# Performance work log

Measured on AMD Instinct MI355X. Metric: run time of the kernel, lower is better.

## Reference

```python
import jax, jax.numpy as jnp
import numpy as np

N = 50000          # num nodes
E = 256            # expert_hidden_dim
H = 512            # hidden_dim (expert output / GNN dim)
NE = 5             # num experts: action, spatial, temporal, semantic, safety
K = 2              # top_k
GH = 128           # gating hidden dim
EDGES = 800000
L = 2              # gnn layers
TEMP = 1.0


def setup_inputs() -> dict:
    key = jax.random.key(0)
    ks = jax.random.split(key, 16)
    s = 0.02
    inp = {
        "text": jax.random.normal(ks[0], (N, E), jnp.float32),
        "tabular": jax.random.normal(ks[1], (N, E), jnp.float32),
        "structured": jax.random.normal(ks[2], (N, E), jnp.float32),
        "edge_index": jax.random.randint(ks[3], (2, EDGES), 0, N, jnp.int64),
        # gating MLP: [3E] -> GH -> NE
        "Wg1": jax.random.normal(ks[4], (3 * E, GH), jnp.float32) * s,
        "bg1": jnp.zeros((GH,), jnp.float32),
        "Wg2": jax.random.normal(ks[5], (GH, NE), jnp.float32) * s,
        "bg2": jnp.zeros((NE,), jnp.float32),
        # 5 expert MLPs (stacked): E -> H -> H
        "We1": jax.random.normal(ks[6], (NE, E, H), jnp.float32) * s,
        "be1": jnp.zeros((NE, H), jnp.float32),
        "We2": jax.random.normal(ks[7], (NE, H, H), jnp.float32) * s,
        "be2": jnp.zeros((NE, H), jnp.float32),
        # GNN per-layer self/neighbor transforms
        "Wself": jax.random.normal(ks[8], (L, H, H), jnp.float32) * s,
        "Wnbr": jax.random.normal(ks[9], (L, H, H), jnp.float32) * s,
    }
    return inp


def _moe_gnn(text, tabular, structured, edge_index,
             Wg1, bg1, Wg2, bg2, We1, be1, We2, be2, Wself, Wnbr):
    # ---- gating: softmax over experts, top-k, renormalize ----
    combined = jnp.concatenate([text, tabular, structured], axis=-1)  # [N, 3E]
    g = jax.nn.relu(combined @ Wg1 + bg1)
    logits = (g @ Wg2 + bg2) / TEMP                                   # [N, NE]
    probs = jax.nn.softmax(logits, axis=-1)
    top_vals, top_idx = jax.lax.top_k(probs, K)                       # [N, K]
    gates = top_vals / jnp.sum(top_vals, axis=-1, keepdims=True)      # [N, K]

    # ---- expert inputs per the forward() mapping ----
    # action->tabular, spatial->structured, temporal->text, semantic->text, safety->structured
    xin = jnp.stack([tabular, structured, text, text, structured])    # [NE, N, E]

    # ---- expert MLPs (all experts computed densely, selected by gather) ----
    h1 = jax.nn.gelu(jnp.einsum('end,edh->enh', xin, We1) + be1[:, None, :])
    eout = jnp.einsum('enh,eho->eno', h1, We2) + be2[:, None, :]      # [NE, N, H]

    # ---- gather-dispatch-scatter: weighted sum of top-k expert outputs ----
    sel = eout[top_idx, jnp.arange(N)[:, None], :]                    # [N, K, H]
    node_feats = jnp.sum(gates[..., None] * sel, axis=1)              # [N, H]

    # ---- GNN message passing over edge list ----
    src, dst = edge_index[0], edge_index[1]
    h = node_feats
    for l in range(L):
        msg = jax.ops.segment_sum((h @ Wnbr[l])[src], dst, num_segments=N)
        h = jax.nn.relu(h @ Wself[l] + msg)
    return h


def reference(text, tabular, structured, edge_index,
              Wg1, bg1, Wg2, bg2, We1, be1, We2, be2, Wself, Wnbr):
    return _moe_gnn(text, tabular, structured, edge_index,
                    Wg1, bg1, Wg2, bg2, We1, be1, We2, be2, Wself, Wnbr)
```

## Files before the change

kernel.cpp:

```cpp
#include <hip/hip_runtime.h>
#include <hip/hip_bf16.h>

#define NNODE 50000
#define M_PAD 50048
#define EDIM  256
#define HDIM  512
#define NEXP  5
#define GHID  128
#define NEDGE 800000
#define SLOTCAP 101504
#define MAXT_ALL 792
#define MAXT_R   396

typedef __attribute__((ext_vector_type(8))) short  short8;
typedef __attribute__((ext_vector_type(4))) float  float4v;
typedef __attribute__((ext_vector_type(4))) unsigned short ushort4v;

typedef __attribute__((address_space(1))) const unsigned int gas_u32;
typedef __attribute__((address_space(3))) unsigned int       las_u32;

__device__ __forceinline__ void gl_lds16(const unsigned short* g, unsigned short* l) {
    __builtin_amdgcn_global_load_lds((gas_u32*)g, (las_u32*)l, 16, 0, 0);
}
__device__ __forceinline__ unsigned short f2b(float f) {
    unsigned u = __builtin_bit_cast(unsigned, f);
    u += 0x7FFFu + ((u >> 16) & 1u);
    return (unsigned short)(u >> 16);
}
__device__ __forceinline__ float b2f(unsigned short h) {
    unsigned u = ((unsigned)h) << 16;
    return __builtin_bit_cast(float, u);
}
__device__ __forceinline__ float fast_tanh(float y) {
    float ay = fabsf(y);
    float e  = __expf(-2.0f * ay);
    float t  = (1.0f - e) / (1.0f + e);
    return (y < 0.0f) ? -t : t;
}
__device__ __forceinline__ float gelu_tanh(float x) {
    float inner = 0.7978845608028654f * (x + 0.044715f * x * x * x);
    return 0.5f * x * (1.0f + fast_tanh(inner));
}

#define WP_N0 655360
#define WP_C1 1966080
#define WP_C2 3014656
#define WP_TOT 3112960
#define WP_T_RL  WP_TOT
#define WP_T_DEG (WP_TOT + SLOTCAP)
#define WP_T_SC  (WP_TOT + SLOTCAP + NNODE)
#define WP_ALL   (WP_TOT + SLOTCAP + NNODE + 16)
__global__ __launch_bounds__(256) void wprep(
    const float* __restrict__ We1, const float* __restrict__ We2,
    const float* __restrict__ Wself, const float* __restrict__ Wnbr,
    const float* __restrict__ Wg1,
    unsigned short* __restrict__ We1t, unsigned short* __restrict__ We2t,
    unsigned short* __restrict__ Wcat0, unsigned short* __restrict__ Wcat1,
    unsigned short* __restrict__ Wg1h, unsigned short* __restrict__ Wg1l,
    int* __restrict__ rowlist, int* __restrict__ deg, int* __restrict__ slotcnt) {
    for (int i = blockIdx.x * blockDim.x + threadIdx.x; i < WP_ALL;
         i += gridDim.x * blockDim.x) {
        if (i < WP_N0) {
            int b = i >> 17, rem = i & 131071;
            int c = rem >> 8, r = rem & 255;
            We1t[i] = f2b(We1[(size_t)b * 131072 + (size_t)r * 512 + c]);
        } else if (i < WP_C1) {
            int j = i - WP_N0;
            int b = j >> 18, rem = j & 262143;
            int c = rem >> 9, r = rem & 511;
            We2t[j] = f2b(We2[(size_t)b * 262144 + (size_t)r * 512 + c]);
        } else if (i < WP_C2) {
            int j = i - WP_C1;
            int qd = j >> 18, k = j & 262143;
            int c = k >> 9, r = k & 511;
            const float* in = (qd & 1) ? Wnbr : Wself;
            if (qd >> 1) in += 262144;
            unsigned short* out = (qd >> 1) ? Wcat1 : Wcat0;
            int ko = (qd & 1) * 512;
            out[(size_t)c * 1024 + ko + r] = f2b(in[(size_t)r * 512 + c]);
        } else if (i < WP_TOT) {
            int j = i - WP_C2;
            int c = j / 768, r = j - c * 768;
            float f = Wg1[(size_t)r * 128 + c];
            unsigned short hi = f2b(f);
            Wg1h[j] = hi;
            Wg1l[j] = f2b(f - b2f(hi));
        } else if (i < WP_T_DEG) {
            rowlist[i - WP_T_RL] = -1;
        } else if (i < WP_T_SC) {
            deg[i - WP_T_DEG] = 0;
        } else {
            slotcnt[i - WP_T_SC] = 0;
        }
    }
}

__global__ __launch_bounds__(256) void gate128(
    const float* __restrict__ xtxt, const float* __restrict__ xtab, const float* __restrict__ xstr,
    const unsigned short* __restrict__ Bh, const unsigned short* __restrict__ Blo,
    const float* __restrict__ bg1, float* __restrict__ g) {
    __shared__ unsigned short Ash[128 * 64];
    __shared__ unsigned short Asl[128 * 64];
    __shared__ unsigned short Bsh[128 * 64];
    __shared__ unsigned short Bsl[128 * 64];
    const int t = threadIdx.x, w = t >> 6, lane = t & 63;
    const int ln = lane & 15, q = lane >> 4;
    const int wm = (w >> 1) * 64, wn = (w & 1) * 64;
    const int rb = w * 8 + (lane >> 3), kg = lane & 7;
    const int koff = (kg ^ (rb & 7)) * 8;
    const float* xs[3] = { xtxt, xtab, xstr };
    const unsigned short* Bgh = Bh  + (size_t)rb * 768 + koff;
    const unsigned short* Bgl = Blo + (size_t)rb * 768 + koff;
    unsigned short* Blh = &Bsh[rb * 64 + kg * 8];
    unsigned short* Bll = &Bsl[rb * 64 + kg * 8];
    float4v acc[4][4];
#pragma unroll
    for (int i = 0; i < 4; ++i)
#pragma unroll
        for (int j = 0; j < 4; ++j) acc[i][j] = (float4v){0.f, 0.f, 0.f, 0.f};

    for (int kt = 0; kt < 768; kt += 64) {
        const float* xp = xs[kt >> 8];
        const int kloc = kt & 255;
        __syncthreads();
#pragma unroll
        for (int it = 0; it < 4; ++it) {
            int row = blockIdx.y * 128 + rb + 32 * it;
            union { short8 v; unsigned short s[8]; } ph, pl;
            if (row < NNODE) {
                const float* sp = xp + (size_t)row * EDIM + kloc + koff;
                float4v a0 = *(const float4v*)sp;
                float4v a1 = *(const float4v*)(sp + 4);
#pragma unroll
                for (int c = 0; c < 4; ++c) {
                    unsigned short h0 = f2b(a0[c]);
                    ph.s[c] = h0; pl.s[c] = f2b(a0[c] - b2f(h0));
                    unsigned short h1 = f2b(a1[c]);
                    ph.s[4 + c] = h1; pl.s[4 + c] = f2b(a1[c] - b2f(h1));
                }
            } else {
#pragma unroll
                for (int c = 0; c < 8; ++c) { ph.s[c] = 0; pl.s[c] = 0; }
            }
            *(short8*)&Ash[(rb + 32 * it) * 64 + kg * 8] = ph.v;
            *(short8*)&Asl[(rb + 32 * it) * 64 + kg * 8] = pl.v;
            gl_lds16(Bgh + (size_t)it * 32 * 768 + kt, Blh + it * 32 * 64);
            gl_lds16(Bgl + (size_t)it * 32 * 768 + kt, Bll + it * 32 * 64);
        }
        __syncthreads();
#pragma unroll
        for (int kk = 0; kk < 2; ++kk) {
            short8 ah[4], al[4], bh[4], bl[4];
#pragma unroll
            for (int i = 0; i < 4; ++i) {
                int off = (wm + 16 * i + ln) * 64 + (((kk * 4 + q) ^ (ln & 7)) * 8);
                ah[i] = *(const short8*)&Ash[off];
                al[i] = *(const short8*)&Asl[off];
            }
#pragma unroll
            for (int j = 0; j < 4; ++j) {
                int off = (wn + 16 * j + ln) * 64 + (((kk * 4 + q) ^ (ln & 7)) * 8);
                bh[j] = *(const short8*)&Bsh[off];
                bl[j] = *(const short8*)&Bsl[off];
            }
#pragma unroll
            for (int i = 0; i < 4; ++i)
#pragma unroll
                for (int j = 0; j < 4; ++j) {
                    acc[i][j] = __builtin_amdgcn_mfma_f32_16x16x32_bf16(ah[i], bh[j], acc[i][j], 0, 0, 0);
                    acc[i][j] = __builtin_amdgcn_mfma_f32_16x16x32_bf16(ah[i], bl[j], acc[i][j], 0, 0, 0);
                    acc[i][j] = __builtin_amdgcn_mfma_f32_16x16x32_bf16(al[i], bh[j], acc[i][j], 0, 0, 0);
                }
        }
    }
    const int gm0 = blockIdx.y * 128 + wm;
#pragma unroll
    for (int i = 0; i < 4; ++i)
#pragma unroll
        for (int j = 0; j < 4; ++j) {
            int gn = wn + 16 * j + ln;
            float bc = bg1[gn];
#pragma unroll
            for (int r = 0; r < 4; ++r) {
                int gm = gm0 + 16 * i + q * 4 + r;
                g[(size_t)gm * GHID + gn] = fmaxf(acc[i][j][r] + bc, 0.f);
            }
        }
}

__global__ __launch_bounds__(256) void gating(
    const float* __restrict__ g, const float* __restrict__ Wg2, const float* __restrict__ bg2,
    float* __restrict__ gates, int* __restrict__ esel) {
    int wv = threadIdx.x >> 6, lane = threadIdx.x & 63;
    int n = blockIdx.x * 4 + wv;
    float p[NEXP];
    float g1 = g[(size_t)n * GHID + lane];
    float g2 = g[(size_t)n * GHID + 64 + lane];
#pragma unroll
    for (int e = 0; e < NEXP; ++e)
        p[e] = g1 * Wg2[lane * NEXP + e] + g2 * Wg2[(64 + lane) * NEXP + e];
#pragma unroll
    for (int off = 32; off > 0; off >>= 1)
#pragma unroll
        for (int e = 0; e < NEXP; ++e) p[e] += __shfl_xor(p[e], off, 64);
    if (lane == 0) {
        float l[NEXP], mx = -1e30f;
#pragma unroll
        for (int e = 0; e < NEXP; ++e) { l[e] = p[e] + bg2[e]; mx = fmaxf(mx, l[e]); }
        float pr[NEXP], s = 0.f;
#pragma unroll
        for (int e = 0; e < NEXP; ++e) { pr[e] = expf(l[e] - mx); s += pr[e]; }
#pragma unroll
        for (int e = 0; e < NEXP; ++e) pr[e] /= s;
        int i0 = 0;
#pragma unroll
        for (int e = 1; e < NEXP; ++e) if (pr[e] > pr[i0]) i0 = e;
        int i1 = -1;
#pragma unroll
        for (int e = 0; e < NEXP; ++e) if (e != i0 && (i1 < 0 || pr[e] > pr[i1])) i1 = e;
        float v0 = pr[i0], v1 = pr[i1], s2 = v0 + v1;
        gates[2 * n]     = v0 / s2;
        gates[2 * n + 1] = v1 / s2;
        esel[2 * n]      = i0;
        esel[2 * n + 1]  = i1;
    }
}

__global__ __launch_bounds__(256) void slot_count(const int* __restrict__ esel,
                                                  int* __restrict__ slotcnt) {
    __shared__ int h[10];
    if (threadIdx.x < 10) h[threadIdx.x] = 0;
    __syncthreads();
    int n = blockIdx.x * 256 + threadIdx.x;
    if (n < NNODE) {
        atomicAdd(&h[esel[2 * n] * 2 + 0], 1);
        atomicAdd(&h[esel[2 * n + 1] * 2 + 1], 1);
    }
    __syncthreads();
    if (threadIdx.x < 10) atomicAdd(&slotcnt[threadIdx.x], h[threadIdx.x]);
}
__global__ void seg_plan(const int* __restrict__ slotcnt, int* __restrict__ cursor,
                         int* __restrict__ header, int2* __restrict__ meta_all,
                         int2* __restrict__ meta_r0, int2* __restrict__ meta_r1) {
    if (threadIdx.x == 0 && blockIdx.x == 0) {
        int base = 0, ta = 0, t0 = 0, t1 = 0;
        for (int s = 0; s < 10; ++s) {
            cursor[s] = base;
            int nt = (slotcnt[s] + 127) >> 7;
            for (int k = 0; k < nt; ++k) {
                int2 m; m.x = s; m.y = base + k * 128;
                meta_all[ta++] = m;
                if (s & 1) meta_r1[t1++] = m; else meta_r0[t0++] = m;
            }
            base += nt * 128;
        }
        header[0] = ta; header[1] = t0; header[2] = t1;
    }
}
__global__ __launch_bounds__(256) void slot_fill(
    const int* __restrict__ esel, const float* __restrict__ gates, int* __restrict__ cursor,
    int* __restrict__ rowlist, float* __restrict__ gateval) {
    __shared__ int h[10], base[10];
    if (threadIdx.x < 10) h[threadIdx.x] = 0;
    __syncthreads();
    int n = blockIdx.x * 256 + threadIdx.x;
    int s0 = 0, s1 = 0, p0 = 0, p1 = 0;
    bool on = (n < NNODE);
    if (on) {
        s0 = esel[2 * n] * 2;
        s1 = esel[2 * n + 1] * 2 + 1;
        p0 = atomicAdd(&h[s0], 1);
        p1 = atomicAdd(&h[s1], 1);
    }
    __syncthreads();
    if (threadIdx.x < 10) base[threadIdx.x] = atomicAdd(&cursor[threadIdx.x], h[threadIdx.x]);
    __syncthreads();
    if (on) {
        int q0 = base[s0] + p0, q1 = base[s1] + p1;
        rowlist[q0] = n; gateval[q0] = gates[2 * n];
        rowlist[q1] = n; gateval[q1] = gates[2 * n + 1];
    }
}

__global__ __launch_bounds__(256) void gemm_moe1(
    const float* __restrict__ xtab, const float* __restrict__ xstr, const float* __restrict__ xtxt,
    const unsigned short* __restrict__ We1t, const float* __restrict__ be1,
    const int* __restrict__ header, const int2* __restrict__ meta,
    const int* __restrict__ rowlist, unsigned short* __restrict__ h1) {
    const int wg = blockIdx.x;
    const int xcd = wg & 7, s = wg >> 3;
    const int mt_i = (s >> 2) * 8 + xcd;
    const int ntile = s & 3;
    if (mt_i >= header[0]) return;
    __shared__ unsigned short As[128 * 64];
    __shared__ unsigned short Bs[128 * 64];
    int2 mt = meta[mt_i];
    const int eid = mt.x >> 1, rowbase = mt.y;
    const float* xf = (eid == 0) ? xtab : ((eid == 1 || eid == 4) ? xstr : xtxt);
    const int t = threadIdx.x, w = t >> 6, lane = t & 63;
    const int ln = lane & 15, q = lane >> 4;
    const int wm = (w >> 1) * 64, wn = (w & 1) * 64;
    const int rb = w * 8 + (lane >> 3), kg = lane & 7;
    const int koff = (kg ^ (rb & 7)) * 8;
    int rows[4];
#pragma unroll
    for (int it = 0; it < 4; ++it) {
        int rr = rowlist[rowbase + rb + 32 * it];
        rows[it] = (rr < 0) ? 0 : rr;
    }
    const unsigned short* Bg = We1t + (size_t)eid * HDIM * EDIM
                             + (size_t)(ntile * 128 + rb) * EDIM + koff;
    unsigned short* Bl = &Bs[rb * 64 + kg * 8];
    float4v acc[4][4];
#pragma unroll
    for (int i = 0; i < 4; ++i)
#pragma unroll
        for (int j = 0; j < 4; ++j) acc[i][j] = (float4v){0.f, 0.f, 0.f, 0.f};

    for (int kt = 0; kt < EDIM; kt += 64) {
        __syncthreads();
#pragma unroll
        for (int it = 0; it < 4; ++it) {
            const float* sp = xf + (size_t)rows[it] * EDIM + kt + koff;
            float4v a0 = *(const float4v*)sp;
            float4v a1 = *(const float4v*)(sp + 4);
            union { short8 v; unsigned short s[8]; } pk;
#pragma unroll
            for (int c = 0; c < 4; ++c) { pk.s[c] = f2b(a0[c]); pk.s[4 + c] = f2b(a1[c]); }
            *(short8*)&As[(rb + 32 * it) * 64 + kg * 8] = pk.v;
            gl_lds16(Bg + (size_t)it * 32 * EDIM + kt, Bl + it * 32 * 64);
        }
        __syncthreads();
#pragma unroll
        for (int kk = 0; kk < 2; ++kk) {
            short8 af[4], bf[4];
#pragma unroll
            for (int i = 0; i < 4; ++i)
                af[i] = *(const short8*)&As[(wm + 16 * i + ln) * 64 + (((kk * 4 + q) ^ (ln & 7)) * 8)];
#pragma unroll
            for (int j = 0; j < 4; ++j)
                bf[j] = *(const short8*)&Bs[(wn + 16 * j + ln) * 64 + (((kk * 4 + q) ^ (ln & 7)) * 8)];
#pragma unroll
            for (int i = 0; i < 4; ++i)
#pragma unroll
                for (int j = 0; j < 4; ++j)
                    acc[i][j] = __builtin_amdgcn_mfma_f32_16x16x32_bf16(af[i], bf[j], acc[i][j], 0, 0, 0);
        }
    }
    const int gn0 = ntile * 128 + wn;
#pragma unroll
    for (int i = 0; i < 4; ++i)
#pragma unroll
        for (int j = 0; j < 4; ++j) {
            int gn = gn0 + 16 * j + ln;
            float bc = be1[eid * HDIM + gn];
#pragma unroll
            for (int r = 0; r < 4; ++r) {
                int slot = rowbase + wm + 16 * i + q * 4 + r;
                h1[(size_t)slot * HDIM + gn] = f2b(gelu_tanh(acc[i][j][r] + bc));
            }
        }
}

template<int RMW>
__global__ __launch_bounds__(256) void gemm_moe2(
    const unsigned short* __restrict__ h1, const unsigned short* __restrict__ We2t,
    const float* __restrict__ be2, const int* __restrict__ header,
    const int2* __restrict__ meta, const int* __restrict__ rowlist,
    const float* __restrict__ gateval, unsigned short* __restrict__ nf) {
    const int wg = blockIdx.x;
    const int xcd = wg & 7, s = wg >> 3;
    const int mt_i = (s >> 2) * 8 + xcd;
    const int ntile = s & 3;
    if (mt_i >= header[RMW ? 2 : 1]) return;
    __shared__ unsigned short As[128 * 64];
    __shared__ unsigned short Bs[128 * 64];
    int2 mt = meta[mt_i];
    const int eid = mt.x >> 1, rowbase = mt.y;
    const int t = threadIdx.x, w = t >> 6, lane = t & 63;
    const int ln = lane & 15, q = lane >> 4;
    const int wm = (w >> 1) * 64, wn = (w & 1) * 64;
    const int rb = w * 8 + (lane >> 3), kg = lane & 7;
    const int koff = (kg ^ (rb & 7)) * 8;
    const unsigned short* Ag = h1 + (size_t)(rowbase + rb) * HDIM + koff;
    const unsigned short* Bg = We2t + (size_t)eid * HDIM * HDIM
                             + (size_t)(ntile * 128 + rb) * HDIM + koff;
    unsigned short* Al = &As[rb * 64 + kg * 8];
    unsigned short* Bl = &Bs[rb * 64 + kg * 8];
    float4v acc[4][4];
#pragma unroll
    for (int i = 0; i < 4; ++i)
#pragma unroll
        for (int j = 0; j < 4; ++j) acc[i][j] = (float4v){0.f, 0.f, 0.f, 0.f};

    for (int kt = 0; kt < HDIM; kt += 64) {
        __syncthreads();
#pragma unroll
        for (int it = 0; it < 4; ++it) {
            gl_lds16(Ag + (size_t)it * 32 * HDIM + kt, Al + it * 32 * 64);
            gl_lds16(Bg + (size_t)it * 32 * HDIM + kt, Bl + it * 32 * 64);
        }
        __syncthreads();
#pragma unroll
        for (int kk = 0; kk < 2; ++kk) {
            short8 af[4], bf[4];
#pragma unroll
            for (int i = 0; i < 4; ++i)
                af[i] = *(const short8*)&As[(wm + 16 * i + ln) * 64 + (((kk * 4 + q) ^ (ln & 7)) * 8)];
#pragma unroll
            for (int j = 0; j < 4; ++j)
                bf[j] = *(const short8*)&Bs[(wn + 16 * j + ln) * 64 + (((kk * 4 + q) ^ (ln & 7)) * 8)];
#pragma unroll
            for (int i = 0; i < 4; ++i)
#pragma unroll
                for (int j = 0; j < 4; ++j)
                    acc[i][j] = __builtin_amdgcn_mfma_f32_16x16x32_bf16(af[i], bf[j], acc[i][j], 0, 0, 0);
        }
    }
    const int gn0 = ntile * 128 + wn;
#pragma unroll
    for (int i = 0; i < 4; ++i)
#pragma unroll
        for (int r = 0; r < 4; ++r) {
            int slot = rowbase + wm + 16 * i + q * 4 + r;
            int node = rowlist[slot];
            if (node >= 0) {
                float gt = gateval[slot];
#pragma unroll
                for (int j = 0; j < 4; ++j) {
                    int gn = gn0 + 16 * j + ln;
                    size_t o = (size_t)node * HDIM + gn;
                    float v = gt * (acc[i][j][r] + be2[eid * HDIM + gn]);
                    nf[o] = RMW ? f2b(b2f(nf[o]) + v) : f2b(v);
                }
            }
        }
}

#define GNN_MT (M_PAD / 128)
template<int FINAL>
__global__ __launch_bounds__(256) void gemm_gnn(
    const unsigned short* __restrict__ A0, const unsigned short* __restrict__ A1,
    const unsigned short* __restrict__ Bt, unsigned short* __restrict__ Cb,
    float* __restrict__ Cf) {
    const int wg = blockIdx.x;
    const int xcd = wg & 7, s = wg >> 3;
    const int mt = (s >> 2) * 8 + xcd;
    const int ntile = s & 3;
    if (mt >= GNN_MT) return;
    __shared__ unsigned short As[128 * 64];
    __shared__ unsigned short Bs[128 * 64];
    const int t = threadIdx.x, w = t >> 6, lane = t & 63;
    const int ln = lane & 15, q = lane >> 4;
    const int wm = (w >> 1) * 64, wn = (w & 1) * 64;
    const int rb = w * 8 + (lane >> 3), kg = lane & 7;
    const int koff = (kg ^ (rb & 7)) * 8;
    const unsigned short* Ag0 = A0 + (size_t)(mt * 128 + rb) * HDIM + koff;
    const unsigned short* Ag1 = A1 + (size_t)(mt * 128 + rb) * HDIM + koff;
    const unsigned short* Bg  = Bt + (size_t)(ntile * 128 + rb) * 1024 + koff;
    unsigned short* Al = &As[rb * 64 + kg * 8];
    unsigned short* Bl = &Bs[rb * 64 + kg * 8];
    float4v acc[4][4];
#pragma unroll
    for (int i = 0; i < 4; ++i)
#pragma unroll
        for (int j = 0; j < 4; ++j) acc[i][j] = (float4v){0.f, 0.f, 0.f, 0.f};

    for (int kt = 0; kt < 1024; kt += 64) {
        __syncthreads();
#pragma unroll
        for (int it = 0; it < 4; ++it) {
            const unsigned short* asrc = (kt < HDIM)
                ? (Ag0 + (size_t)it * 32 * HDIM + kt)
                : (Ag1 + (size_t)it * 32 * HDIM + (kt - HDIM));
            gl_lds16(asrc, Al + it * 32 * 64);
            gl_lds16(Bg + (size_t)it * 32 * 1024 + kt, Bl + it * 32 * 64);
        }
        __syncthreads();
#pragma unroll
        for (int kk = 0; kk < 2; ++kk) {
            short8 af[4], bf[4];
#pragma unroll
            for (int i = 0; i < 4; ++i)
                af[i] = *(const short8*)&As[(wm + 16 * i + ln) * 64 + (((kk * 4 + q) ^ (ln & 7)) * 8)];
#pragma unroll
            for (int j = 0; j < 4; ++j)
                bf[j] = *(const short8*)&Bs[(wn + 16 * j + ln) * 64 + (((kk * 4 + q) ^ (ln & 7)) * 8)];
#pragma unroll
            for (int i = 0; i < 4; ++i)
#pragma unroll
                for (int j = 0; j < 4; ++j)
                    acc[i][j] = __builtin_amdgcn_mfma_f32_16x16x32_bf16(af[i], bf[j], acc[i][j], 0, 0, 0);
        }
    }
    const int gm0 = mt * 128 + wm;
    const int gn0 = ntile * 128 + wn;
#pragma unroll
    for (int i = 0; i < 4; ++i)
#pragma unroll
        for (int j = 0; j < 4; ++j) {
            int gn = gn0 + 16 * j + ln;
#pragma unroll
            for (int r = 0; r < 4; ++r) {
                int gm = gm0 + 16 * i + q * 4 + r;
                float v = fmaxf(acc[i][j][r], 0.f);
                if (FINAL) {
                    if (gm < NNODE) Cf[(size_t)gm * HDIM + gn] = v;
                } else {
                    Cb[(size_t)gm * HDIM + gn] = f2b(v);
                }
            }
        }
}

__global__ void hist_kernel(const int* __restrict__ dst, int* __restrict__ deg) {
    int i = blockIdx.x * blockDim.x + threadIdx.x;
    if (i < NEDGE) atomicAdd(&deg[dst[i]], 1);
}
__global__ void scan_block(const int* __restrict__ in, int* __restrict__ incl,
                           int* __restrict__ bsum, int n) {
    __shared__ int s[256];
    int i = blockIdx.x * 256 + threadIdx.x;
    s[threadIdx.x] = (i < n) ? in[i] : 0;
    __syncthreads();
    for (int off = 1; off < 256; off <<= 1) {
        int t = (threadIdx.x >= (unsigned)off) ? s[threadIdx.x - off] : 0;
        __syncthreads();
        s[threadIdx.x] += t;
        __syncthreads();
    }
    if (i < n) incl[i] = s[threadIdx.x];
    if (bsum != nullptr && threadIdx.x == 255) bsum[blockIdx.x] = s[255];
}
__global__ void scan_fix(const int* __restrict__ incl, const int* __restrict__ deg,
                         const int* __restrict__ bscan, int* __restrict__ rowstart,
                         int* __restrict__ ecur) {
    int i = blockIdx.x * blockDim.x + threadIdx.x;
    if (i < NNODE) {
        int b = i >> 8;
        int add = (b > 0) ? bscan[b - 1] : 0;
        int st = incl[i] - deg[i] + add;
        rowstart[i] = st;
        ecur[i] = st;
    }
}
__global__ void fill_csr(const int* __restrict__ src, const int* __restrict__ dst,
                         int* __restrict__ ecur, int* __restrict__ srcs) {
    int e = blockIdx.x * blockDim.x + threadIdx.x;
    if (e < NEDGE) {
        int pos = atomicAdd(&ecur[dst[e]], 1);
        srcs[pos] = src[e];
    }
}

__global__ __launch_bounds__(256) void msg_sum_w(
    const unsigned short* __restrict__ h, const int* __restrict__ rowstart,
    const int* __restrict__ deg, const int* __restrict__ srcs,
    unsigned short* __restrict__ agg) {
    const int wv = threadIdx.x >> 6, lane = threadIdx.x & 63;
    const int n = blockIdx.x * 4 + wv;
    const int st = rowstart[n], d = deg[n];
    float acc[8] = {0.f,0.f,0.f,0.f,0.f,0.f,0.f,0.f};
    const unsigned short* hp = h + (size_t)lane * 8;
    for (int cb = 0; cb < d; cb += 64) {
        int cnt = d - cb; if (cnt > 64) cnt = 64;
        int sidx = (cb + lane < d) ? srcs[st + cb + lane] : 0;
        int t = 0;
        for (; t + 4 <= cnt; t += 4) {
            int s0 = __shfl(sidx, t,     64);
            int s1 = __shfl(sidx, t + 1, 64);
            int s2 = __shfl(sidx, t + 2, 64);
            int s3 = __shfl(sidx, t + 3, 64);
            short8 v0 = *(const short8*)(hp + (size_t)s0 * HDIM);
            short8 v1 = *(const short8*)(hp + (size_t)s1 * HDIM);
            short8 v2 = *(const short8*)(hp + (size_t)s2 * HDIM);
            short8 v3 = *(const short8*)(hp + (size_t)s3 * HDIM);
#pragma unroll
            for (int c = 0; c < 8; ++c)
                acc[c] += (b2f((unsigned short)v0[c]) + b2f((unsigned short)v1[c]))
                        + (b2f((unsigned short)v2[c]) + b2f((unsigned short)v3[c]));
        }
        for (; t < cnt; ++t) {
            int s = __shfl(sidx, t, 64);
            short8 v = *(const short8*)(hp + (size_t)s * HDIM);
#pragma unroll
            for (int c = 0; c < 8; ++c) acc[c] += b2f((unsigned short)v[c]);
        }
    }
    union { short8 v; unsigned short s[8]; } o;
#pragma unroll
    for (int c = 0; c < 8; ++c) o.s[c] = f2b(acc[c]);
    *(short8*)(agg + (size_t)n * HDIM + lane * 8) = o.v;
}

extern "C" void kernel_launch(void* const* d_in, const int* in_sizes, int n_in,
                              void* d_out, int out_size, void* d_ws, size_t ws_size,
                              hipStream_t stream) {
    (void)in_sizes; (void)n_in; (void)out_size; (void)ws_size;
    const float* text       = (const float*)d_in[0];
    const float* tabular    = (const float*)d_in[1];
    const float* structured = (const float*)d_in[2];
    const int*   e_in       = (const int*)d_in[3];
    const float* Wg1  = (const float*)d_in[4];
    const float* bg1  = (const float*)d_in[5];
    const float* Wg2  = (const float*)d_in[6];
    const float* bg2  = (const float*)d_in[7];
    const float* We1  = (const float*)d_in[8];
    const float* be1  = (const float*)d_in[9];
    const float* We2  = (const float*)d_in[10];
    const float* be2  = (const float*)d_in[11];
    const float* Wself = (const float*)d_in[12];
    const float* Wnbr  = (const float*)d_in[13];
    const int* src = e_in;
    const int* dst = e_in + NEDGE;
    float* dout = (float*)d_out;

    char* w = (char*)d_ws;
    auto alloc = [&](size_t bytes) { char* p = w; w += (bytes + 511) & ~(size_t)511; return p; };
    const size_t SZ_H = (size_t)M_PAD * HDIM * 2;
    unsigned short* We1t  = (unsigned short*)alloc((size_t)NEXP * HDIM * EDIM * 2);
    unsigned short* We2t  = (unsigned short*)alloc((size_t)NEXP * HDIM * HDIM * 2);
    unsigned short* Wcat0 = (unsigned short*)alloc((size_t)HDIM * 1024 * 2);
    unsigned short* Wcat1 = (unsigned short*)alloc((size_t)HDIM * 1024 * 2);
    unsigned short* Wg1h  = (unsigned short*)alloc((size_t)GHID * 768 * 2);
    unsigned short* Wg1l  = (unsigned short*)alloc((size_t)GHID * 768 * 2);
    float* gates    = (float*)alloc((size_t)NNODE * 2 * 4);
    int*   esel     = (int*)alloc((size_t)NNODE * 2 * 4);
    int*   slotcnt  = (int*)alloc(16 * 4);
    int*   scursor  = (int*)alloc(16 * 4);
    int*   header   = (int*)alloc(16 * 4);
    int2*  meta_all = (int2*)alloc((size_t)MAXT_ALL * 8);
    int2*  meta_r0  = (int2*)alloc((size_t)MAXT_R * 8);
    int2*  meta_r1  = (int2*)alloc((size_t)MAXT_R * 8);
    int*   rowlist  = (int*)alloc((size_t)SLOTCAP * 4);
    float* gateval  = (float*)alloc((size_t)SLOTCAP * 4);
    int*   deg      = (int*)alloc((size_t)NNODE * 4);
    int*   incl     = (int*)alloc((size_t)NNODE * 4);
    int*   bsum     = (int*)alloc(1024 * 4);
    int*   bscan    = (int*)alloc(1024 * 4);
    int*   rowstart = (int*)alloc((size_t)NNODE * 4);
    int*   ecur     = (int*)alloc((size_t)NNODE * 4);
    int*   srcs     = (int*)alloc((size_t)NEDGE * 4);
    unsigned short* nfb = (unsigned short*)alloc(SZ_H);
    char* regA = alloc((size_t)M_PAD * GHID * 4 > SZ_H ? (size_t)M_PAD * GHID * 4 : SZ_H);
    float*          gbuf = (float*)regA;
    unsigned short* aggb = (unsigned short*)regA;
    char* regB = alloc((size_t)SLOTCAP * HDIM * 2);
    unsigned short* h1c = (unsigned short*)regB;
    unsigned short* hb  = (unsigned short*)regB;

    wprep<<<1024, 256, 0, stream>>>(We1, We2, Wself, Wnbr, Wg1,
                                    We1t, We2t, Wcat0, Wcat1, Wg1h, Wg1l,
                                    rowlist, deg, slotcnt);

    gate128<<<dim3(1, M_PAD / 128), 256, 0, stream>>>(text, tabular, structured,
                                                      Wg1h, Wg1l, bg1, gbuf);
    gating<<<NNODE / 4, 256, 0, stream>>>(gbuf, Wg2, bg2, gates, esel);

    slot_count<<<(NNODE + 255) / 256, 256, 0, stream>>>(esel, slotcnt);
    seg_plan<<<1, 64, 0, stream>>>(slotcnt, scursor, header, meta_all, meta_r0, meta_r1);
    slot_fill<<<(NNODE + 255) / 256, 256, 0, stream>>>(esel, gates, scursor, rowlist, gateval);

    gemm_moe1<<<MAXT_ALL * 4, 256, 0, stream>>>(
        tabular, structured, text, We1t, be1, header, meta_all, rowlist, h1c);
    gemm_moe2<0><<<8 * 50 * 4, 256, 0, stream>>>(
        h1c, We2t, be2, header, meta_r0, rowlist, gateval, nfb);
    gemm_moe2<1><<<8 * 50 * 4, 256, 0, stream>>>(
        h1c, We2t, be2, header, meta_r1, rowlist, gateval, nfb);

    const int NB = (NNODE + 255) / 256;
    hist_kernel<<<(NEDGE + 255) / 256, 256, 0, stream>>>(dst, deg);
    scan_block<<<NB, 256, 0, stream>>>(deg, incl, bsum, NNODE);
    scan_block<<<1, 256, 0, stream>>>(bsum, bscan, nullptr, NB);
    scan_fix<<<NB, 256, 0, stream>>>(incl, deg, bscan, rowstart, ecur);
    fill_csr<<<(NEDGE + 255) / 256, 256, 0, stream>>>(src, dst, ecur, srcs);

    msg_sum_w<<<NNODE / 4, 256, 0, stream>>>(nfb, rowstart, deg, srcs, aggb);
    gemm_gnn<0><<<8 * 49 * 4, 256, 0, stream>>>(nfb, aggb, Wcat0, hb, nullptr);

    msg_sum_w<<<NNODE / 4, 256, 0, stream>>>(hb, rowstart, deg, srcs, aggb);
    gemm_gnn<1><<<8 * 49 * 4, 256, 0, stream>>>(hb, aggb, Wcat1, nullptr, dout);
}
```

Baseline: 1.048 ms.

## Bucket CSR edges by source quarter and split gather by feature slice per XCD

Builds the CSR with four buckets per destination node, keyed by which quarter of the source-node range the edge comes from. The neighbour-sum kernel then walks the quarters in order and assigns 128-column feature slices to XCD pairs, so each gather phase touches a smaller, more cache-resident slice of h. The aim is better L2/MALL hit rates on the random gathers. The cost is a 4x larger degree/scan array, a new second-level scan kernel, serial per-thread edge loops with less memory-level parallelism, and a dependence on blocks being dispatched round-robin across XCDs.

```diff
diff --git a/kernel.cpp b/kernel.cpp
--- a/kernel.cpp
+++ b/kernel.cpp
@@ -41,6 +41,9 @@
     float inner = 0.7978845608028654f * (x + 0.044715f * x * x * x);
     return 0.5f * x * (1.0f + fast_tanh(inner));
 }
+__device__ __forceinline__ int quarter(int s) {
+    return (s >= 25000) ? ((s >= 37500) ? 3 : 2) : ((s >= 12500) ? 1 : 0);
+}
 
 #define WP_N0 655360
 #define WP_C1 1966080
@@ -48,8 +51,8 @@
 #define WP_TOT 3112960
 #define WP_T_RL  WP_TOT
 #define WP_T_DEG (WP_TOT + SLOTCAP)
-#define WP_T_SC  (WP_TOT + SLOTCAP + NNODE)
-#define WP_ALL   (WP_TOT + SLOTCAP + NNODE + 16)
+#define WP_T_SC  (WP_TOT + SLOTCAP + 4 * NNODE)
+#define WP_ALL   (WP_TOT + SLOTCAP + 4 * NNODE + 16)
 __global__ __launch_bounds__(256) void wprep(
     const float* __restrict__ We1, const float* __restrict__ We2,
     const float* __restrict__ Wself, const float* __restrict__ Wnbr,
@@ -57,7 +60,7 @@
     unsigned short* __restrict__ We1t, unsigned short* __restrict__ We2t,
     unsigned short* __restrict__ Wcat0, unsigned short* __restrict__ Wcat1,
     unsigned short* __restrict__ Wg1h, unsigned short* __restrict__ Wg1l,
-    int* __restrict__ rowlist, int* __restrict__ deg, int* __restrict__ slotcnt) {
+    int* __restrict__ rowlist, int* __restrict__ deg4, int* __restrict__ slotcnt) {
     for (int i = blockIdx.x * blockDim.x + threadIdx.x; i < WP_ALL;
          i += gridDim.x * blockDim.x) {
         if (i < WP_N0) {
@@ -88,7 +91,7 @@
         } else if (i < WP_T_DEG) {
             rowlist[i - WP_T_RL] = -1;
         } else if (i < WP_T_SC) {
-            deg[i - WP_T_DEG] = 0;
+            deg4[i - WP_T_DEG] = 0;
         } else {
             slotcnt[i - WP_T_SC] = 0;
         }
@@ -513,9 +516,10 @@
         }
 }
 
-__global__ void hist_kernel(const int* __restrict__ dst, int* __restrict__ deg) {
+__global__ void hist4(const int* __restrict__ src, const int* __restrict__ dst,
+                      int* __restrict__ deg4) {
     int i = blockIdx.x * blockDim.x + threadIdx.x;
-    if (i < NEDGE) atomicAdd(&deg[dst[i]], 1);
+    if (i < NEDGE) atomicAdd(&deg4[4 * dst[i] + quarter(src[i])], 1);
 }
 __global__ void scan_block(const int* __restrict__ in, int* __restrict__ incl,
                            int* __restrict__ bsum, int n) {
@@ -532,65 +536,92 @@
     if (i < n) incl[i] = s[threadIdx.x];
     if (bsum != nullptr && threadIdx.x == 255) bsum[blockIdx.x] = s[255];
 }
-__global__ void scan_fix(const int* __restrict__ incl, const int* __restrict__ deg,
-                         const int* __restrict__ bscan, int* __restrict__ rowstart,
-                         int* __restrict__ ecur) {
+__global__ void scan_lvl2(const int* __restrict__ in, int* __restrict__ out, int n) {
+    __shared__ int s[1024];
+    int i = threadIdx.x;
+    s[i] = (i < n) ? in[i] : 0;
+    __syncthreads();
+    for (int off = 1; off < 1024; off <<= 1) {
+        int t = (i >= (unsigned)off) ? s[i - off] : 0;
+        __syncthreads();
+        s[i] += t;
+        __syncthreads();
+    }
+    if (i < n) out[i] = s[i];
+}
+__global__ void scan_fix4(const int* __restrict__ incl, const int* __restrict__ deg4,
+                          const int* __restrict__ bscan, int* __restrict__ rowstart4,
+                          int* __restrict__ ecur4, int n) {
     int i = blockIdx.x * blockDim.x + threadIdx.x;
-    if (i < NNODE) {
+    if (i < n) {
         int b = i >> 8;
         int add = (b > 0) ? bscan[b - 1] : 0;
-        int st = incl[i] - deg[i] + add;
-        rowstart[i] = st;
-        ecur[i] = st;
-    }
-}
-__global__ void fill_csr(const int* __restrict__ src, const int* __restrict__ dst,
-                         int* __restrict__ ecur, int* __restrict__ srcs) {
+        int st = incl[i] - deg4[i] + add;
+        rowstart4[i] = st;
+        ecur4[i] = st;
+    }
+}
+__global__ void fill_csr4(const int* __restrict__ src, const int* __restrict__ dst,
+                          int* __restrict__ ecur4, int* __restrict__ srcs) {
     int e = blockIdx.x * blockDim.x + threadIdx.x;
     if (e < NEDGE) {
-        int pos = atomicAdd(&ecur[dst[e]], 1);
-        srcs[pos] = src[e];
-    }
-}
-
-__global__ __launch_bounds__(256) void msg_sum_w(
-    const unsigned short* __restrict__ h, const int* __restrict__ rowstart,
-    const int* __restrict__ deg, const int* __restrict__ srcs,
+        int s = src[e];
+        int pos = atomicAdd(&ecur4[4 * dst[e] + quarter(s)], 1);
+        srcs[pos] = s;
+    }
+}
+
+#define MSQ_NPB 64
+#define MSQ_CHUNKS ((NNODE + MSQ_NPB - 1) / MSQ_NPB)
+#define MSQ_GRID (8 * ((MSQ_CHUNKS + 1) / 2))
+__global__ __launch_bounds__(256) void msg_sum_q(
+    const unsigned short* __restrict__ h, const int* __restrict__ rowstart4,
+    const int* __restrict__ deg4, const int* __restrict__ srcs,
     unsigned short* __restrict__ agg) {
-    const int wv = threadIdx.x >> 6, lane = threadIdx.x & 63;
-    const int n = blockIdx.x * 4 + wv;
-    const int st = rowstart[n], d = deg[n];
-    float acc[8] = {0.f,0.f,0.f,0.f,0.f,0.f,0.f,0.f};
-    const unsigned short* hp = h + (size_t)lane * 8;
-    for (int cb = 0; cb < d; cb += 64) {
-        int cnt = d - cb; if (cnt > 64) cnt = 64;
-        int sidx = (cb + lane < d) ? srcs[st + cb + lane] : 0;
-        int t = 0;
-        for (; t + 4 <= cnt; t += 4) {
-            int s0 = __shfl(sidx, t,     64);
-            int s1 = __shfl(sidx, t + 1, 64);
-            int s2 = __shfl(sidx, t + 2, 64);
-            int s3 = __shfl(sidx, t + 3, 64);
-            short8 v0 = *(const short8*)(hp + (size_t)s0 * HDIM);
-            short8 v1 = *(const short8*)(hp + (size_t)s1 * HDIM);
-            short8 v2 = *(const short8*)(hp + (size_t)s2 * HDIM);
-            short8 v3 = *(const short8*)(hp + (size_t)s3 * HDIM);
-#pragma unroll
-            for (int c = 0; c < 8; ++c)
-                acc[c] += (b2f((unsigned short)v0[c]) + b2f((unsigned short)v1[c]))
-                        + (b2f((unsigned short)v2[c]) + b2f((unsigned short)v3[c]));
-        }
-        for (; t < cnt; ++t) {
-            int s = __shfl(sidx, t, 64);
-            short8 v = *(const short8*)(hp + (size_t)s * HDIM);
-#pragma unroll
-            for (int c = 0; c < 8; ++c) acc[c] += b2f((unsigned short)v[c]);
-        }
-    }
-    union { short8 v; unsigned short s[8]; } o;
-#pragma unroll
-    for (int c = 0; c < 8; ++c) o.s[c] = f2b(acc[c]);
-    *(short8*)(agg + (size_t)n * HDIM + lane * 8) = o.v;
+    const int blk = blockIdx.x;
+    const int xcd = blk & 7, j = blk >> 3;
+    const int slice = xcd >> 1;
+    const int chunk = j * 2 + (xcd & 1);
+    if (chunk >= MSQ_CHUNKS) return;
+    const int slot = threadIdx.x >> 4;
+    const int slane = threadIdx.x & 15;
+    const int nbase = chunk * MSQ_NPB;
+    const unsigned short* hs = h + slice * 128 + slane * 8;
+    float acc[4][8];
+#pragma unroll
+    for (int d = 0; d < 4; ++d)
+#pragma unroll
+        for (int c = 0; c < 8; ++c) acc[d][c] = 0.f;
+#pragma unroll 1
+    for (int q = 0; q < 4; ++q) {
+#pragma unroll
+        for (int d = 0; d < 4; ++d) {
+            int n = nbase + d * 16 + slot;
+            if (n >= NNODE) continue;
+            int st = rowstart4[4 * n + q];
+            int dg = deg4[4 * n + q];
+            if (dg <= 0) continue;
+            int s = srcs[st];
+            for (int t = 0; t < dg; ++t) {
+                int snext = (t + 1 < dg) ? srcs[st + t + 1] : 0;
+                short8 v = *(const short8*)(hs + (size_t)s * HDIM);
+#pragma unroll
+                for (int c = 0; c < 8; ++c) acc[d][c] += b2f((unsigned short)v[c]);
+                s = snext;
+            }
+        }
+    }
+#pragma unroll
+    for (int d = 0; d < 4; ++d) {
+        int n = nbase + d * 16 + slot;
+        if (n < NNODE) {
+            union { short8 v; unsigned short s[8]; } o;
+#pragma unroll
+            for (int c = 0; c < 8; ++c) o.s[c] = f2b(acc[d][c]);
+            __builtin_nontemporal_store(o.v,
+                (short8*)(agg + (size_t)n * HDIM + slice * 128 + slane * 8));
+        }
+    }
 }
 
 extern "C" void kernel_launch(void* const* d_in, const int* in_sizes, int n_in,
@@ -634,12 +665,12 @@
     int2*  meta_r1  = (int2*)alloc((size_t)MAXT_R * 8);
     int*   rowlist  = (int*)alloc((size_t)SLOTCAP * 4);
     float* gateval  = (float*)alloc((size_t)SLOTCAP * 4);
-    int*   deg      = (int*)alloc((size_t)NNODE * 4);
-    int*   incl     = (int*)alloc((size_t)NNODE * 4);
+    int*   deg4     = (int*)alloc((size_t)4 * NNODE * 4);
+    int*   incl     = (int*)alloc((size_t)4 * NNODE * 4);
     int*   bsum     = (int*)alloc(1024 * 4);
     int*   bscan    = (int*)alloc(1024 * 4);
-    int*   rowstart = (int*)alloc((size_t)NNODE * 4);
-    int*   ecur     = (int*)alloc((size_t)NNODE * 4);
+    int*   rowstart4= (int*)alloc((size_t)4 * NNODE * 4);
+    int*   ecur4    = (int*)alloc((size_t)4 * NNODE * 4);
     int*   srcs     = (int*)alloc((size_t)NEDGE * 4);
     unsigned short* nfb = (unsigned short*)alloc(SZ_H);
     char* regA = alloc((size_t)M_PAD * GHID * 4 > SZ_H ? (size_t)M_PAD * GHID * 4 : SZ_H);
@@ -651,7 +682,7 @@
 
     wprep<<<1024, 256, 0, stream>>>(We1, We2, Wself, Wnbr, Wg1,
                                     We1t, We2t, Wcat0, Wcat1, Wg1h, Wg1l,
-                                    rowlist, deg, slotcnt);
+                                    rowlist, deg4, slotcnt);
 
     gate128<<<dim3(1, M_PAD / 128), 256, 0, stream>>>(text, tabular, structured,
                                                       Wg1h, Wg1l, bg1, gbuf);
@@ -668,16 +699,17 @@
     gemm_moe2<1><<<8 * 50 * 4, 256, 0, stream>>>(
         h1c, We2t, be2, header, meta_r1, rowlist, gateval, nfb);
 
-    const int NB = (NNODE + 255) / 256;
-    hist_kernel<<<(NEDGE + 255) / 256, 256, 0, stream>>>(dst, deg);
-    scan_block<<<NB, 256, 0, stream>>>(deg, incl, bsum, NNODE);
-    scan_block<<<1, 256, 0, stream>>>(bsum, bscan, nullptr, NB);
-    scan_fix<<<NB, 256, 0, stream>>>(incl, deg, bscan, rowstart, ecur);
-    fill_csr<<<(NEDGE + 255) / 256, 256, 0, stream>>>(src, dst, ecur, srcs);
-
-    msg_sum_w<<<NNODE / 4, 256, 0, stream>>>(nfb, rowstart, deg, srcs, aggb);
+    const int N4  = 4 * NNODE;
+    const int NB4 = (N4 + 255) / 256;
+    hist4<<<(NEDGE + 255) / 256, 256, 0, stream>>>(src, dst, deg4);
+    scan_block<<<NB4, 256, 0, stream>>>(deg4, incl, bsum, N4);
+    scan_lvl2<<<1, 1024, 0, stream>>>(bsum, bscan, NB4);
+    scan_fix4<<<NB4, 256, 0, stream>>>(incl, deg4, bscan, rowstart4, ecur4, N4);
+    fill_csr4<<<(NEDGE + 255) / 256, 256, 0, stream>>>(src, dst, ecur4, srcs);
+
+    msg_sum_q<<<MSQ_GRID, 256, 0, stream>>>(nfb, rowstart4, deg4, srcs, aggb);
     gemm_gnn<0><<<8 * 49 * 4, 256, 0, stream>>>(nfb, aggb, Wcat0, hb, nullptr);
 
-    msg_sum_w<<<NNODE / 4, 256, 0, stream>>>(hb, rowstart, deg, srcs, aggb);
+    msg_sum_q<<<MSQ_GRID, 256, 0, stream>>>(hb, rowstart4, deg4, srcs, aggb);
     gemm_gnn<1><<<8 * 49 * 4, 256, 0, stream>>>(hb, aggb, Wcat1, nullptr, dout);
 }
```

Result: slower. 1.138 ms (+8.5%).

## Fuse gating MLP, softmax top-k and slot counting into one kernel

Applied to the files above, without the earlier changes.

The first gating layer result is now staged in shared memory instead of a global buffer. The same block then computes the second layer, softmax, top-2 selection and the per-slot histogram. This removes the global write and read of the N x 128 hidden tensor and two kernel launches. In exchange the block needs about 66 KB of shared memory, which may lower occupancy, and the epilogue runs a serial per-row loop of 32 rows per wave.

```diff
diff --git a/kernel.cpp b/kernel.cpp
--- a/kernel.cpp
+++ b/kernel.cpp
@@ -95,19 +95,25 @@
     }
 }
 
-__global__ __launch_bounds__(256) void gate128(
+__global__ __launch_bounds__(256) void gate_fused(
     const float* __restrict__ xtxt, const float* __restrict__ xtab, const float* __restrict__ xstr,
     const unsigned short* __restrict__ Bh, const unsigned short* __restrict__ Blo,
-    const float* __restrict__ bg1, float* __restrict__ g) {
-    __shared__ unsigned short Ash[128 * 64];
-    __shared__ unsigned short Asl[128 * 64];
-    __shared__ unsigned short Bsh[128 * 64];
-    __shared__ unsigned short Bsl[128 * 64];
+    const float* __restrict__ bg1, const float* __restrict__ Wg2,
+    const float* __restrict__ bg2, float* __restrict__ gates,
+    int* __restrict__ esel, int* __restrict__ slotcnt) {
+    __shared__ __align__(16) char smem[66096];
+    unsigned short* Ash = (unsigned short*)smem;
+    unsigned short* Asl = Ash + 128 * 64;
+    unsigned short* Bsh = Asl + 128 * 64;
+    unsigned short* Bsl = Bsh + 128 * 64;
+    float* gsm = (float*)smem;
+    int*   hcnt = (int*)(smem + 66048);
     const int t = threadIdx.x, w = t >> 6, lane = t & 63;
     const int ln = lane & 15, q = lane >> 4;
     const int wm = (w >> 1) * 64, wn = (w & 1) * 64;
     const int rb = w * 8 + (lane >> 3), kg = lane & 7;
     const int koff = (kg ^ (rb & 7)) * 8;
+    if (t < 10) hcnt[t] = 0;
     const float* xs[3] = { xtxt, xtab, xstr };
     const unsigned short* Bgh = Bh  + (size_t)rb * 768 + koff;
     const unsigned short* Bgl = Blo + (size_t)rb * 768 + koff;
@@ -173,7 +179,7 @@
                 }
         }
     }
-    const int gm0 = blockIdx.y * 128 + wm;
+    __syncthreads();
 #pragma unroll
     for (int i = 0; i < 4; ++i)
 #pragma unroll
@@ -181,64 +187,59 @@
             int gn = wn + 16 * j + ln;
             float bc = bg1[gn];
 #pragma unroll
-            for (int r = 0; r < 4; ++r) {
-                int gm = gm0 + 16 * i + q * 4 + r;
-                g[(size_t)gm * GHID + gn] = fmaxf(acc[i][j][r] + bc, 0.f);
-            }
-        }
-}
-
-__global__ __launch_bounds__(256) void gating(
-    const float* __restrict__ g, const float* __restrict__ Wg2, const float* __restrict__ bg2,
-    float* __restrict__ gates, int* __restrict__ esel) {
-    int wv = threadIdx.x >> 6, lane = threadIdx.x & 63;
-    int n = blockIdx.x * 4 + wv;
-    float p[NEXP];
-    float g1 = g[(size_t)n * GHID + lane];
-    float g2 = g[(size_t)n * GHID + 64 + lane];
-#pragma unroll
-    for (int e = 0; e < NEXP; ++e)
-        p[e] = g1 * Wg2[lane * NEXP + e] + g2 * Wg2[(64 + lane) * NEXP + e];
-#pragma unroll
-    for (int off = 32; off > 0; off >>= 1)
-#pragma unroll
-        for (int e = 0; e < NEXP; ++e) p[e] += __shfl_xor(p[e], off, 64);
-    if (lane == 0) {
-        float l[NEXP], mx = -1e30f;
-#pragma unroll
-        for (int e = 0; e < NEXP; ++e) { l[e] = p[e] + bg2[e]; mx = fmaxf(mx, l[e]); }
-        float pr[NEXP], s = 0.f;
-#pragma unroll
-        for (int e = 0; e < NEXP; ++e) { pr[e] = expf(l[e] - mx); s += pr[e]; }
-#pragma unroll
-        for (int e = 0; e < NEXP; ++e) pr[e] /= s;
-        int i0 = 0;
-#pragma unroll
-        for (int e = 1; e < NEXP; ++e) if (pr[e] > pr[i0]) i0 = e;
-        int i1 = -1;
-#pragma unroll
-        for (int e = 0; e < NEXP; ++e) if (e != i0 && (i1 < 0 || pr[e] > pr[i1])) i1 = e;
-        float v0 = pr[i0], v1 = pr[i1], s2 = v0 + v1;
-        gates[2 * n]     = v0 / s2;
-        gates[2 * n + 1] = v1 / s2;
-        esel[2 * n]      = i0;
-        esel[2 * n + 1]  = i1;
-    }
-}
-
-__global__ __launch_bounds__(256) void slot_count(const int* __restrict__ esel,
-                                                  int* __restrict__ slotcnt) {
-    __shared__ int h[10];
-    if (threadIdx.x < 10) h[threadIdx.x] = 0;
+            for (int r = 0; r < 4; ++r)
+                gsm[(wm + 16 * i + q * 4 + r) * 129 + gn] = fmaxf(acc[i][j][r] + bc, 0.f);
+        }
     __syncthreads();
-    int n = blockIdx.x * 256 + threadIdx.x;
-    if (n < NNODE) {
-        atomicAdd(&h[esel[2 * n] * 2 + 0], 1);
-        atomicAdd(&h[esel[2 * n + 1] * 2 + 1], 1);
+    float wg_a[NEXP], wg_b[NEXP], bgl[NEXP];
+#pragma unroll
+    for (int e = 0; e < NEXP; ++e) {
+        wg_a[e] = Wg2[lane * NEXP + e];
+        wg_b[e] = Wg2[(64 + lane) * NEXP + e];
+        bgl[e]  = bg2[e];
+    }
+    const int row0 = w * 32;
+#pragma unroll 1
+    for (int k = 0; k < 32; ++k) {
+        int lrow = row0 + k;
+        int n = blockIdx.y * 128 + lrow;
+        float g1 = gsm[lrow * 129 + lane];
+        float g2 = gsm[lrow * 129 + 64 + lane];
+        float p[NEXP];
+#pragma unroll
+        for (int e = 0; e < NEXP; ++e) p[e] = g1 * wg_a[e] + g2 * wg_b[e];
+#pragma unroll
+        for (int off = 32; off > 0; off >>= 1)
+#pragma unroll
+            for (int e = 0; e < NEXP; ++e) p[e] += __shfl_xor(p[e], off, 64);
+        if (lane == 0 && n < NNODE) {
+            float l[NEXP], mx = -1e30f;
+#pragma unroll
+            for (int e = 0; e < NEXP; ++e) { l[e] = p[e] + bgl[e]; mx = fmaxf(mx, l[e]); }
+            float pr[NEXP], s = 0.f;
+#pragma unroll
+            for (int e = 0; e < NEXP; ++e) { pr[e] = expf(l[e] - mx); s += pr[e]; }
+#pragma unroll
+            for (int e = 0; e < NEXP; ++e) pr[e] /= s;
+            int i0 = 0;
+#pragma unroll
+            for (int e = 1; e < NEXP; ++e) if (pr[e] > pr[i0]) i0 = e;
+            int i1 = -1;
+#pragma unroll
+            for (int e = 0; e < NEXP; ++e) if (e != i0 && (i1 < 0 || pr[e] > pr[i1])) i1 = e;
+            float v0 = pr[i0], v1 = pr[i1], s2 = v0 + v1;
+            gates[2 * n]     = v0 / s2;
+            gates[2 * n + 1] = v1 / s2;
+            esel[2 * n]      = i0;
+            esel[2 * n + 1]  = i1;
+            atomicAdd(&hcnt[i0 * 2 + 0], 1);
+            atomicAdd(&hcnt[i1 * 2 + 1], 1);
+        }
     }
     __syncthreads();
-    if (threadIdx.x < 10) atomicAdd(&slotcnt[threadIdx.x], h[threadIdx.x]);
-}
+    if (t < 10) atomicAdd(&slotcnt[t], hcnt[t]);
+}
+
 __global__ void seg_plan(const int* __restrict__ slotcnt, int* __restrict__ cursor,
                          int* __restrict__ header, int2* __restrict__ meta_all,
                          int2* __restrict__ meta_r0, int2* __restrict__ meta_r1) {
@@ -643,7 +644,6 @@
     int*   srcs     = (int*)alloc((size_t)NEDGE * 4);
     unsigned short* nfb = (unsigned short*)alloc(SZ_H);
     char* regA = alloc((size_t)M_PAD * GHID * 4 > SZ_H ? (size_t)M_PAD * GHID * 4 : SZ_H);
-    float*          gbuf = (float*)regA;
     unsigned short* aggb = (unsigned short*)regA;
     char* regB = alloc((size_t)SLOTCAP * HDIM * 2);
     unsigned short* h1c = (unsigned short*)regB;
@@ -653,11 +653,9 @@
                                     We1t, We2t, Wcat0, Wcat1, Wg1h, Wg1l,
                                     rowlist, deg, slotcnt);
 
-    gate128<<<dim3(1, M_PAD / 128), 256, 0, stream>>>(text, tabular, structured,
-                                                      Wg1h, Wg1l, bg1, gbuf);
-    gating<<<NNODE / 4, 256, 0, stream>>>(gbuf, Wg2, bg2, gates, esel);
-
-    slot_count<<<(NNODE + 255) / 256, 256, 0, stream>>>(esel, slotcnt);
+    gate_fused<<<dim3(1, M_PAD / 128), 256, 0, stream>>>(
+        text, tabular, structured, Wg1h, Wg1l, bg1, Wg2, bg2, gates, esel, slotcnt);
+
     seg_plan<<<1, 64, 0, stream>>>(slotcnt, scursor, header, meta_all, meta_r0, meta_r1);
     slot_fill<<<(NNODE + 255) / 256, 256, 0, stream>>>(esel, gates, scursor, rowlist, gateval);
 
```

Result: no change. 1.049 ms (+0.1%).
